# Performance work log

Measured on AMD Instinct MI355X. Metric: run time of the kernel, lower is better.

## Reference

```python
import jax, jax.numpy as jnp
import numpy as np

N, D, E, EDGE_DIM, HID4 = 8192, 128, 262144, 50, 32


def setup_inputs() -> dict:
    key = jax.random.key(0)
    k = jax.random.split(key, 8)
    return {
        "mag": jax.random.uniform(k[0], (N, D), dtype=jnp.float32),
        "phase": jax.random.normal(k[1], (N, D), dtype=jnp.float32),
        "edge_index": jax.random.randint(k[2], (2, E), 0, N, dtype=jnp.int64),
        "rbf": jax.random.uniform(k[3], (E, EDGE_DIM), dtype=jnp.float32),
        "W1": jax.random.normal(k[4], (EDGE_DIM, HID4), dtype=jnp.float32) * 0.1,
        "b1": jnp.zeros((HID4,), dtype=jnp.float32),
        "W2": jax.random.normal(k[5], (HID4, 1), dtype=jnp.float32) * 0.1,
        "b2": jnp.zeros((1,), dtype=jnp.float32),
    }


def reference(mag, phase, edge_index, rbf, W1, b1, W2, b2):
    # score_ij = sum_d |z_i||z_j| cos(theta_i - theta_j) / sqrt(D)
    # cos(a-b) identity: = (mag*cos(phase)) @ (mag*cos(phase))^T + (mag*sin)@(mag*sin)^T
    scale = jnp.sqrt(jnp.asarray(mag.shape[-1], mag.dtype))
    a = mag * jnp.cos(phase)  # [N, D]
    b = mag * jnp.sin(phase)  # [N, D]
    scores = (a @ a.T + b @ b.T) / scale  # [N, N]
    # edge bias: Linear -> SiLU -> Linear -> scalar, scattered onto (i, j)
    h = jax.nn.silu(rbf @ W1 + b1)       # [E, HID4]
    bias = (h @ W2 + b2)[:, 0]           # [E]
    scores = scores.at[edge_index[0], edge_index[1]].add(bias)
    attn = jax.nn.softmax(scores, axis=1)  # softmax over keys j
    new_mag = attn @ mag
    new_phase = attn @ phase
    return new_mag, new_phase
```

## Files before the change

kernel.cpp:

```cpp
#include <hip/hip_runtime.h>
#include <hip/hip_bf16.h>

#define NN 8192
#define DD 128
#define DQK 256
#define EE 262144
#define EDGE_DIM 50
#define HID 32
#define CAP 96
#define SCALE 0.08838834764831845f
#define SCALE_LOG2E 0.12752455522410585f

using f32x4 = __attribute__((ext_vector_type(4))) float;
using f32x2 = __attribute__((ext_vector_type(2))) float;
using bf16x8 = __attribute__((ext_vector_type(8))) short;
using s16x4 = __attribute__((ext_vector_type(4))) short;

static __device__ __forceinline__ short f2b(float f) {
  __hip_bfloat16 h = __float2bfloat16(f);
  return __builtin_bit_cast(short, h);
}
static __device__ __forceinline__ float b2f(short s) {
  unsigned u = ((unsigned)(unsigned short)s) << 16;
  return __builtin_bit_cast(float, u);
}

__global__ __launch_bounds__(256) void k1_prep(const float* __restrict__ mag,
                                               const float* __restrict__ phase,
                                               short* __restrict__ qkb,
                                               short* __restrict__ vtb,
                                               int* __restrict__ cnt) {
  __shared__ float tile[64][65];
  int b = blockIdx.x;
  int tid = threadIdx.x;
  if (b < 4096) {
    int t = b * 256 + tid;
    int n = t >> 7, d = t & 127;
    float m = mag[t], p = phase[t];
    float sn, cs;
    __sincosf(p, &sn, &cs);
    qkb[(size_t)n * DQK + d] = f2b(m * cs);
    qkb[(size_t)n * DQK + 128 + d] = f2b(m * sn);
    return;
  }
  if (b < 4608) {
    int r = b - 4096;
    int bn = r & 127, bd = (r >> 7) & 1, sel = r >> 8;
    const float* src = sel ? phase : mag;
#pragma unroll
    for (int rep = 0; rep < 16; ++rep) {
      int idx = rep * 256 + tid;
      int rr = idx >> 6, c = idx & 63;
      tile[rr][c] = src[(size_t)(bn * 64 + rr) * DD + bd * 64 + c];
    }
    __syncthreads();
#pragma unroll
    for (int rep = 0; rep < 16; ++rep) {
      int idx = rep * 256 + tid;
      int rr = idx >> 6, c = idx & 63;
      vtb[(size_t)(sel * 128 + bd * 64 + rr) * NN + bn * 64 + c] = f2b(tile[c][rr]);
    }
    return;
  }
  int r = b - 4608;
  cnt[r * 256 + tid] = 0;
}

__global__ __launch_bounds__(256) void k2_mlp(
    const float* __restrict__ rbf, const float* __restrict__ W1,
    const float* __restrict__ b1, const float* __restrict__ W2,
    const float* __restrict__ b2, const int* __restrict__ eidx,
    float* __restrict__ bias, int* __restrict__ cnt, int* __restrict__ slot) {
  __shared__ alignas(16) float w1s[EDGE_DIM * HID];
  __shared__ alignas(16) float b1s[HID];
  __shared__ alignas(16) float w2s[HID];
  __shared__ float b2s;
  int tid = threadIdx.x;
  for (int k = tid; k < EDGE_DIM * HID; k += 256) w1s[k] = W1[k];
  if (tid < HID) { b1s[tid] = b1[tid]; w2s[tid] = W2[tid]; }
  if (tid == 0) b2s = b2[0];
  __syncthreads();
  int e = blockIdx.x * 256 + tid;
  const float* rrow = rbf + (size_t)e * EDGE_DIM;
  f32x4 r4[12];
#pragma unroll
  for (int k = 0; k < 12; ++k) r4[k] = *reinterpret_cast<const f32x4*>(rrow + 4 * k);
  f32x2 rt = *reinterpret_cast<const f32x2*>(rrow + 48);
  f32x4 h[8];
#pragma unroll
  for (int jj = 0; jj < 8; ++jj) h[jj] = reinterpret_cast<const f32x4*>(b1s)[jj];
#pragma unroll
  for (int k = 0; k < 12; ++k) {
#pragma unroll
    for (int qq = 0; qq < 4; ++qq) {
      const f32x4* wrow = reinterpret_cast<const f32x4*>(w1s + (4 * k + qq) * HID);
#pragma unroll
      for (int jj = 0; jj < 8; ++jj) h[jj] += r4[k][qq] * wrow[jj];
    }
  }
  {
    const f32x4* w48 = reinterpret_cast<const f32x4*>(w1s + 48 * HID);
    const f32x4* w49 = reinterpret_cast<const f32x4*>(w1s + 49 * HID);
#pragma unroll
    for (int jj = 0; jj < 8; ++jj) h[jj] += rt.x * w48[jj] + rt.y * w49[jj];
  }
  float outv = b2s;
#pragma unroll
  for (int jj = 0; jj < 8; ++jj) {
    f32x4 x = h[jj];
    f32x4 sl;
#pragma unroll
    for (int q = 0; q < 4; ++q) sl[q] = x[q] / (1.0f + __expf(-x[q]));
    f32x4 pr = sl * reinterpret_cast<const f32x4*>(w2s)[jj];
    outv += pr.x + pr.y + pr.z + pr.w;
  }
  bias[e] = outv;
  int i = eidx[e];
  int p = atomicAdd(&cnt[i], 1);
  if (p < CAP) slot[i * CAP + p] = e;
}

constexpr int TBM = 128;
constexpr int TBN = 128;
constexpr int QP = 264;
constexpr int KP = 72;
constexpr int PP = 136;

template <int NSPLIT>
__global__ __launch_bounds__(512, 2) void k5_flash(
    const short* __restrict__ qk,
    const short* __restrict__ vt,
    float* __restrict__ nump,
    float* __restrict__ denp) {
  constexpr int QCOLS = NN / NSPLIT;
  constexpr int NCHUNK = QCOLS / TBN;
  constexpr int GPQ = 8 / NSPLIT;
  __shared__ short Qs[TBM * QP];
  __shared__ short KV[2 * TBN * KP];
  __shared__ short Ps[TBM * PP];
  __shared__ float dl[4][TBM];
  int b = blockIdx.x;
  int q = (b & 7) / GPQ;
  int rb = (b >> 3) * GPQ + (b & (GPQ - 1));
  int tid = threadIdx.x;
  int w = tid >> 6, lane = tid & 63;
  int wr = w >> 2, wc = w & 3;
  int l15 = lane & 15, quad = lane >> 4;
  int r0 = rb * TBM;
  int cbase = q * QCOLS;

#pragma unroll
  for (int p = 0; p < 8; ++p) {
    int idx = p * 512 + tid;
    int row = idx >> 5, g = idx & 31;
    *(bf16x8*)&Qs[row * QP + g * 8] =
        *(const bf16x8*)(qk + (size_t)(r0 + row) * DQK + g * 8);
  }

  f32x4 o[4][4] = {};
  float den[4][4] = {};
  __syncthreads();

  for (int ch = 0; ch < NCHUNK; ++ch) {
    int c0 = cbase + ch * TBN;
#pragma unroll
    for (int p = 0; p < 2; ++p) {
      int idx = p * 512 + tid;
      int col = idx >> 3, g = idx & 7;
      *(bf16x8*)&KV[col * KP + g * 8] =
          *(const bf16x8*)(qk + (size_t)(c0 + col) * DQK + g * 8);
    }
    __syncthreads();
    f32x4 s[4][2] = {};
#pragma unroll
    for (int bk = 0; bk < 4; ++bk) {
      int buf = bk & 1;
      if (bk < 3) {
        int nb = buf ^ 1;
#pragma unroll
        for (int p = 0; p < 2; ++p) {
          int idx = p * 512 + tid;
          int col = idx >> 3, g = idx & 7;
          *(bf16x8*)&KV[nb * (TBN * KP) + col * KP + g * 8] =
              *(const bf16x8*)(qk + (size_t)(c0 + col) * DQK + (bk + 1) * 64 + g * 8);
        }
      }
#pragma unroll
      for (int ks = 0; ks < 2; ++ks) {
        int ko = ks * 32 + quad * 8;
        bf16x8 a[4], bb[2];
#pragma unroll
        for (int rt = 0; rt < 4; ++rt)
          a[rt] = *(const bf16x8*)&Qs[(wr * 64 + rt * 16 + l15) * QP + bk * 64 + ko];
#pragma unroll
        for (int ct = 0; ct < 2; ++ct)
          bb[ct] = *(const bf16x8*)&KV[buf * (TBN * KP) + (wc * 32 + ct * 16 + l15) * KP + ko];
#pragma unroll
        for (int rt = 0; rt < 4; ++rt)
#pragma unroll
          for (int ct = 0; ct < 2; ++ct)
            s[rt][ct] = __builtin_amdgcn_mfma_f32_16x16x32_bf16(a[rt], bb[ct],
                                                                s[rt][ct], 0, 0, 0);
      }
      __syncthreads();
    }
#pragma unroll
    for (int rt = 0; rt < 4; ++rt)
#pragma unroll
      for (int ct = 0; ct < 2; ++ct)
#pragma unroll
        for (int r = 0; r < 4; ++r) {
          float pv = exp2f(s[rt][ct][r] * SCALE_LOG2E);
          den[rt][r] += pv;
          Ps[(wr * 64 + rt * 16 + quad * 4 + r) * PP + wc * 32 + ct * 16 + l15] = f2b(pv);
        }
    __syncthreads();
#pragma unroll
    for (int jb = 0; jb < 2; ++jb) {
#pragma unroll
      for (int p = 0; p < 4; ++p) {
        int idx = p * 512 + tid;
        int feat = idx >> 3, g = idx & 7;
        *(bf16x8*)&KV[feat * KP + g * 8] =
            *(const bf16x8*)(vt + (size_t)feat * NN + c0 + jb * 64 + g * 8);
      }
      __syncthreads();
#pragma unroll
      for (int ks = 0; ks < 2; ++ks) {
        int ko = ks * 32 + quad * 8;
        bf16x8 pa[4], vb[4];
#pragma unroll
        for (int rt = 0; rt < 4; ++rt)
          pa[rt] = *(const bf16x8*)&Ps[(wr * 64 + rt * 16 + l15) * PP + jb * 64 + ko];
#pragma unroll
        for (int ft = 0; ft < 4; ++ft)
          vb[ft] = *(const bf16x8*)&KV[(wc * 64 + ft * 16 + l15) * KP + ko];
#pragma unroll
        for (int rt = 0; rt < 4; ++rt)
#pragma unroll
          for (int ft = 0; ft < 4; ++ft)
            o[rt][ft] = __builtin_amdgcn_mfma_f32_16x16x32_bf16(pa[rt], vb[ft],
                                                                o[rt][ft], 0, 0, 0);
      }
      __syncthreads();
    }
  }
  float* npB = nump + (size_t)q * NN * DQK;
#pragma unroll
  for (int rt = 0; rt < 4; ++rt)
#pragma unroll
    for (int ft = 0; ft < 4; ++ft) {
      int row = r0 + wr * 64 + rt * 16 + quad * 4;
      int feat = wc * 64 + ft * 16 + l15;
#pragma unroll
      for (int r = 0; r < 4; ++r)
        npB[(size_t)(row + r) * DQK + feat] = o[rt][ft][r];
    }
#pragma unroll
  for (int rt = 0; rt < 4; ++rt)
#pragma unroll
    for (int r = 0; r < 4; ++r) {
      float d = den[rt][r];
      d += __shfl_xor(d, 1);
      d += __shfl_xor(d, 2);
      d += __shfl_xor(d, 4);
      d += __shfl_xor(d, 8);
      if (l15 == 0) dl[wc][wr * 64 + rt * 16 + quad * 4 + r] = d;
    }
  __syncthreads();
  if (tid < TBM) {
    float d = dl[0][tid] + dl[1][tid] + dl[2][tid] + dl[3][tid];
    denp[q * NN + r0 + tid] = d;
  }
}

__global__ __launch_bounds__(256) void k6_combine(
    const int* __restrict__ eidx, const float* __restrict__ bias,
    const int* __restrict__ cntArr, const int* __restrict__ slot,
    const short* __restrict__ qk, const float* __restrict__ mag,
    const float* __restrict__ phase, const float* __restrict__ nump,
    const float* __restrict__ denp, float* __restrict__ out, int nsplit) {
  __shared__ short qs[DQK];
  __shared__ int js[CAP];
  __shared__ float bs[CAP];
  __shared__ float ess[CAP];
  __shared__ int keepf[CAP];
  __shared__ f32x4 ncl[4][64];
  __shared__ float dcl[4];
  int i = blockIdx.x;
  int tid = threadIdx.x;
  int wave = tid >> 6;
  int lane = tid & 63;
  int cnt = cntArr[i];
  if (cnt > CAP) cnt = CAP;
  if (tid < DQK) qs[tid] = qk[(size_t)i * DQK + tid];
  for (int p = tid; p < cnt; p += 256) {
    int e = slot[i * CAP + p];
    js[p] = eidx[EE + e];
    bs[p] = bias[e];
  }
  __syncthreads();
  int sub = lane & 7;
  for (int p = wave * 8 + (lane >> 3); p < cnt; p += 32) {
    int j = js[p];
    const bf16x8* kb = reinterpret_cast<const bf16x8*>(qk + (size_t)j * DQK + sub * 32);
    const bf16x8* qa = reinterpret_cast<const bf16x8*>(qs + sub * 32);
    float sp = 0.f;
#pragma unroll
    for (int t = 0; t < 4; ++t) {
      bf16x8 qv = qa[t];
      bf16x8 kv = kb[t];
#pragma unroll
      for (int u = 0; u < 8; ++u) sp += b2f(qv[u]) * b2f(kv[u]);
    }
    sp += __shfl_xor(sp, 1);
    sp += __shfl_xor(sp, 2);
    sp += __shfl_xor(sp, 4);
    if (sub == 0) ess[p] = __expf(sp * SCALE);
  }
  __syncthreads();
  {
    float bsum = 0.f;
    int keep = 0;
    if (tid < cnt) {
      int j = js[tid];
      bsum = bs[tid];
      keep = 1;
      for (int qq = 0; qq < cnt; ++qq) {
        if (qq == tid || js[qq] != j) continue;
        if (qq < tid) { keep = 0; break; }
        bsum += bs[qq];
      }
    }
    __syncthreads();
    if (tid < cnt) { bs[tid] = bsum; keepf[tid] = keep; }
    __syncthreads();
  }
  const float* vbase = (lane < 32) ? (mag + 4 * lane) : (phase + 4 * lane - 128);
  f32x4 nc = {0.f, 0.f, 0.f, 0.f};
  float denc = 0.f;
  if (wave < nsplit) {
    nc = *reinterpret_cast<const f32x4*>(nump + ((size_t)wave * NN + i) * DQK + 4 * lane);
    if (lane == 0) denc = denp[wave * NN + i];
  }
  for (int p = wave; p < cnt; p += 4) {
    if (!keepf[p]) continue;
    float delta = ess[p] * expm1f(bs[p]);
    denc += delta;
    f32x4 v = *reinterpret_cast<const f32x4*>(vbase + (size_t)js[p] * DD);
    nc += delta * v;
  }
  ncl[wave][lane] = nc;
  if (lane == 0) dcl[wave] = denc;
  __syncthreads();
  if (wave == 0) {
    f32x4 nd = ncl[0][lane] + ncl[1][lane] + ncl[2][lane] + ncl[3][lane];
    float den = dcl[0] + dcl[1] + dcl[2] + dcl[3];
    f32x4 res = nd * (1.0f / den);
    if (lane < 32)
      *reinterpret_cast<f32x4*>(out + (size_t)i * DD + 4 * lane) = res;
    else
      *reinterpret_cast<f32x4*>(out + (size_t)NN * DD + (size_t)i * DD + 4 * lane - 128) = res;
  }
}

constexpr size_t OFF_QK = 0;
constexpr size_t OFF_VT = (size_t)NN * DQK * 2;
constexpr size_t OFF_BIAS = OFF_VT + (size_t)DQK * NN * 2;
constexpr size_t OFF_CNT = OFF_BIAS + (size_t)EE * 4;
constexpr size_t OFF_SLOT = OFF_CNT + (size_t)NN * 4;
constexpr size_t OFF_NUMP = (OFF_SLOT + (size_t)NN * CAP * 4 + 255) & ~(size_t)255;
constexpr size_t WS_NEED4 = OFF_NUMP + 4ull * NN * DQK * 4 + 4ull * NN * 4;
constexpr size_t WS_NEED2 = OFF_NUMP + 2ull * NN * DQK * 4 + 2ull * NN * 4;

extern "C" void kernel_launch(void* const* d_in, const int* in_sizes, int n_in,
                              void* d_out, int out_size, void* d_ws, size_t ws_size,
                              hipStream_t stream) {
  const float* mag = (const float*)d_in[0];
  const float* phase = (const float*)d_in[1];
  const int* eidx = (const int*)d_in[2];
  const float* rbf = (const float*)d_in[3];
  const float* W1 = (const float*)d_in[4];
  const float* b1 = (const float*)d_in[5];
  const float* W2 = (const float*)d_in[6];
  const float* b2 = (const float*)d_in[7];
  float* out = (float*)d_out;
  char* ws = (char*)d_ws;
  if (ws_size < WS_NEED2) return;
  int nsplit = (ws_size >= WS_NEED4) ? 4 : 2;

  short* qkb = (short*)(ws + OFF_QK);
  short* vtb = (short*)(ws + OFF_VT);
  float* bias = (float*)(ws + OFF_BIAS);
  int* cnt = (int*)(ws + OFF_CNT);
  int* slot = (int*)(ws + OFF_SLOT);
  float* nump = (float*)(ws + OFF_NUMP);
  float* denp = (float*)(ws + OFF_NUMP + (size_t)nsplit * NN * DQK * 4);

  k1_prep<<<4640, 256, 0, stream>>>(mag, phase, qkb, vtb, cnt);
  k2_mlp<<<EE / 256, 256, 0, stream>>>(rbf, W1, b1, W2, b2, eidx, bias, cnt, slot);
  if (nsplit == 4)
    k5_flash<4><<<(NN / TBM) * 4, 512, 0, stream>>>(qkb, vtb, nump, denp);
  else
    k5_flash<2><<<(NN / TBM) * 2, 512, 0, stream>>>(qkb, vtb, nump, denp);
  k6_combine<<<NN, 256, 0, stream>>>(eidx, bias, cnt, slot, qkb, mag, phase, nump,
                                     denp, out, nsplit);
}
```

Baseline: 314.6 us.

## Use direct global-to-LDS loads with XOR swizzle and merge prep and MLP kernels

The flash kernel's Q, K and V tile loads now use global_load_lds, which writes straight into LDS without a register round trip. Padded LDS strides are replaced with an XOR-swizzled unpadded layout, and the MFMA operand reads apply the matching swizzle to avoid bank conflicts. The prep and edge-MLP kernels are merged into one launch, and the counter zeroing moves to a hipMemsetAsync. This trades register traffic and launch overhead for more complex addressing, and relies on the swizzled layout being correct.

```diff
diff --git a/kernel.cpp b/kernel.cpp
--- a/kernel.cpp
+++ b/kernel.cpp
@@ -24,13 +24,24 @@
   unsigned u = ((unsigned)(unsigned short)s) << 16;
   return __builtin_bit_cast(float, u);
 }
-
-__global__ __launch_bounds__(256) void k1_prep(const float* __restrict__ mag,
-                                               const float* __restrict__ phase,
-                                               short* __restrict__ qkb,
-                                               short* __restrict__ vtb,
-                                               int* __restrict__ cnt) {
+static __device__ __forceinline__ void gll(const short* g, short* l) {
+  __builtin_amdgcn_global_load_lds(
+      (const __attribute__((address_space(1))) void*)g,
+      (__attribute__((address_space(3))) void*)l, 16, 0, 0);
+}
+
+__global__ __launch_bounds__(256) void k1_mega(
+    const float* __restrict__ mag, const float* __restrict__ phase,
+    short* __restrict__ qkb, short* __restrict__ vtb,
+    const float* __restrict__ rbf, const float* __restrict__ W1,
+    const float* __restrict__ b1, const float* __restrict__ W2,
+    const float* __restrict__ b2, const int* __restrict__ eidx,
+    float* __restrict__ bias, int* __restrict__ cnt, int* __restrict__ slot) {
   __shared__ float tile[64][65];
+  __shared__ alignas(16) float w1s[EDGE_DIM * HID];
+  __shared__ alignas(16) float b1s[HID];
+  __shared__ alignas(16) float w2s[HID];
+  __shared__ float b2s;
   int b = blockIdx.x;
   int tid = threadIdx.x;
   if (b < 4096) {
@@ -62,30 +73,16 @@
     }
     return;
   }
-  int r = b - 4608;
-  cnt[r * 256 + tid] = 0;
-}
-
-__global__ __launch_bounds__(256) void k2_mlp(
-    const float* __restrict__ rbf, const float* __restrict__ W1,
-    const float* __restrict__ b1, const float* __restrict__ W2,
-    const float* __restrict__ b2, const int* __restrict__ eidx,
-    float* __restrict__ bias, int* __restrict__ cnt, int* __restrict__ slot) {
-  __shared__ alignas(16) float w1s[EDGE_DIM * HID];
-  __shared__ alignas(16) float b1s[HID];
-  __shared__ alignas(16) float w2s[HID];
-  __shared__ float b2s;
-  int tid = threadIdx.x;
   for (int k = tid; k < EDGE_DIM * HID; k += 256) w1s[k] = W1[k];
   if (tid < HID) { b1s[tid] = b1[tid]; w2s[tid] = W2[tid]; }
   if (tid == 0) b2s = b2[0];
   __syncthreads();
-  int e = blockIdx.x * 256 + tid;
+  int e = (b - 4608) * 256 + tid;
   const float* rrow = rbf + (size_t)e * EDGE_DIM;
   f32x4 r4[12];
 #pragma unroll
   for (int k = 0; k < 12; ++k) r4[k] = *reinterpret_cast<const f32x4*>(rrow + 4 * k);
-  f32x2 rt = *reinterpret_cast<const f32x2*>(rrow + 48);
+  f32x2 rt2 = *reinterpret_cast<const f32x2*>(rrow + 48);
   f32x4 h[8];
 #pragma unroll
   for (int jj = 0; jj < 8; ++jj) h[jj] = reinterpret_cast<const f32x4*>(b1s)[jj];
@@ -102,7 +99,7 @@
     const f32x4* w48 = reinterpret_cast<const f32x4*>(w1s + 48 * HID);
     const f32x4* w49 = reinterpret_cast<const f32x4*>(w1s + 49 * HID);
 #pragma unroll
-    for (int jj = 0; jj < 8; ++jj) h[jj] += rt.x * w48[jj] + rt.y * w49[jj];
+    for (int jj = 0; jj < 8; ++jj) h[jj] += rt2.x * w48[jj] + rt2.y * w49[jj];
   }
   float outv = b2s;
 #pragma unroll
@@ -122,8 +119,6 @@
 
 constexpr int TBM = 128;
 constexpr int TBN = 128;
-constexpr int QP = 264;
-constexpr int KP = 72;
 constexpr int PP = 136;
 
 template <int NSPLIT>
@@ -135,8 +130,8 @@
   constexpr int QCOLS = NN / NSPLIT;
   constexpr int NCHUNK = QCOLS / TBN;
   constexpr int GPQ = 8 / NSPLIT;
-  __shared__ short Qs[TBM * QP];
-  __shared__ short KV[2 * TBN * KP];
+  __shared__ short Qs[TBM * 256];
+  __shared__ short KV[2 * TBN * 64];
   __shared__ short Ps[TBM * PP];
   __shared__ float dl[4][TBM];
   int b = blockIdx.x;
@@ -146,15 +141,17 @@
   int w = tid >> 6, lane = tid & 63;
   int wr = w >> 2, wc = w & 3;
   int l15 = lane & 15, quad = lane >> 4;
+  int rsw = l15 & 7;
+  int wbase = w * 64;
   int r0 = rb * TBM;
   int cbase = q * QCOLS;
 
 #pragma unroll
   for (int p = 0; p < 8; ++p) {
     int idx = p * 512 + tid;
-    int row = idx >> 5, g = idx & 31;
-    *(bf16x8*)&Qs[row * QP + g * 8] =
-        *(const bf16x8*)(qk + (size_t)(r0 + row) * DQK + g * 8);
+    int row = idx >> 5, gs = idx & 31;
+    gll(qk + (size_t)(r0 + row) * DQK + ((gs ^ (row & 7)) * 8),
+        &Qs[(p * 512 + wbase) * 8]);
   }
 
   f32x4 o[4][4] = {};
@@ -166,9 +163,9 @@
 #pragma unroll
     for (int p = 0; p < 2; ++p) {
       int idx = p * 512 + tid;
-      int col = idx >> 3, g = idx & 7;
-      *(bf16x8*)&KV[col * KP + g * 8] =
-          *(const bf16x8*)(qk + (size_t)(c0 + col) * DQK + g * 8);
+      int col = idx >> 3, gs = idx & 7;
+      gll(qk + (size_t)(c0 + col) * DQK + ((gs ^ (col & 7)) * 8),
+          &KV[(p * 512 + wbase) * 8]);
     }
     __syncthreads();
     f32x4 s[4][2] = {};
@@ -180,21 +177,23 @@
 #pragma unroll
         for (int p = 0; p < 2; ++p) {
           int idx = p * 512 + tid;
-          int col = idx >> 3, g = idx & 7;
-          *(bf16x8*)&KV[nb * (TBN * KP) + col * KP + g * 8] =
-              *(const bf16x8*)(qk + (size_t)(c0 + col) * DQK + (bk + 1) * 64 + g * 8);
+          int col = idx >> 3, gs = idx & 7;
+          gll(qk + (size_t)(c0 + col) * DQK + (bk + 1) * 64 + ((gs ^ (col & 7)) * 8),
+              &KV[nb * 8192 + (p * 512 + wbase) * 8]);
         }
       }
 #pragma unroll
       for (int ks = 0; ks < 2; ++ks) {
-        int ko = ks * 32 + quad * 8;
+        int g = ks * 4 + quad;
         bf16x8 a[4], bb[2];
 #pragma unroll
         for (int rt = 0; rt < 4; ++rt)
-          a[rt] = *(const bf16x8*)&Qs[(wr * 64 + rt * 16 + l15) * QP + bk * 64 + ko];
+          a[rt] = *(const bf16x8*)&Qs[(wr * 64 + rt * 16 + l15) * 256 +
+                                      ((bk * 8 + g) ^ rsw) * 8];
 #pragma unroll
         for (int ct = 0; ct < 2; ++ct)
-          bb[ct] = *(const bf16x8*)&KV[buf * (TBN * KP) + (wc * 32 + ct * 16 + l15) * KP + ko];
+          bb[ct] = *(const bf16x8*)&KV[buf * 8192 + (wc * 32 + ct * 16 + l15) * 64 +
+                                       (g ^ rsw) * 8];
 #pragma unroll
         for (int rt = 0; rt < 4; ++rt)
 #pragma unroll
@@ -220,13 +219,14 @@
 #pragma unroll
       for (int p = 0; p < 4; ++p) {
         int idx = p * 512 + tid;
-        int feat = idx >> 3, g = idx & 7;
-        *(bf16x8*)&KV[feat * KP + g * 8] =
-            *(const bf16x8*)(vt + (size_t)feat * NN + c0 + jb * 64 + g * 8);
+        int feat = idx >> 3, gs = idx & 7;
+        gll(vt + (size_t)feat * NN + c0 + jb * 64 + ((gs ^ (feat & 7)) * 8),
+            &KV[(p * 512 + wbase) * 8]);
       }
       __syncthreads();
 #pragma unroll
       for (int ks = 0; ks < 2; ++ks) {
+        int g = ks * 4 + quad;
         int ko = ks * 32 + quad * 8;
         bf16x8 pa[4], vb[4];
 #pragma unroll
@@ -234,7 +234,7 @@
           pa[rt] = *(const bf16x8*)&Ps[(wr * 64 + rt * 16 + l15) * PP + jb * 64 + ko];
 #pragma unroll
         for (int ft = 0; ft < 4; ++ft)
-          vb[ft] = *(const bf16x8*)&KV[(wc * 64 + ft * 16 + l15) * KP + ko];
+          vb[ft] = *(const bf16x8*)&KV[(wc * 64 + ft * 16 + l15) * 64 + (g ^ rsw) * 8];
 #pragma unroll
         for (int rt = 0; rt < 4; ++rt)
 #pragma unroll
@@ -397,8 +397,9 @@
   float* nump = (float*)(ws + OFF_NUMP);
   float* denp = (float*)(ws + OFF_NUMP + (size_t)nsplit * NN * DQK * 4);
 
-  k1_prep<<<4640, 256, 0, stream>>>(mag, phase, qkb, vtb, cnt);
-  k2_mlp<<<EE / 256, 256, 0, stream>>>(rbf, W1, b1, W2, b2, eidx, bias, cnt, slot);
+  hipMemsetAsync(cnt, 0, (size_t)NN * 4, stream);
+  k1_mega<<<5632, 256, 0, stream>>>(mag, phase, qkb, vtb, rbf, W1, b1, W2, b2,
+                                    eidx, bias, cnt, slot);
   if (nsplit == 4)
     k5_flash<4><<<(NN / TBM) * 4, 512, 0, stream>>>(qkb, vtb, nump, denp);
   else
```

Result: faster. 304.8 us (-3.1%).
